# Optimization experiments

Measured on AMD Instinct MI355X. Metric: run time of the kernel, lower is better.

## Reference

```python
import jax, jax.numpy as jnp
import numpy as np

B = 524288
D_IN = 128
D_OUT = 128
MASK_DENSITY = 0.25  # fraction of DAG edges present


def setup_inputs() -> dict:
    key = jax.random.key(0)
    k = jax.random.split(key, 6)
    x0 = jax.random.normal(k[0], (B, D_IN), dtype=jnp.float32)
    x1 = jax.random.normal(k[1], (B, D_IN), dtype=jnp.float32)
    # weights ~ N(0, 0.1^2) as in torch.normal(mean=0, std=0.1)
    w0 = jax.random.normal(k[2], (D_OUT, D_IN), dtype=jnp.float32) * 0.1
    w1 = jax.random.normal(k[3], (D_OUT, D_IN), dtype=jnp.float32) * 0.1
    # binary DAG connectivity masks [out_dim, in_dims[i]]
    m0 = (jax.random.uniform(k[4], (D_OUT, D_IN)) < MASK_DENSITY).astype(jnp.float32)
    m1 = (jax.random.uniform(k[5], (D_OUT, D_IN)) < MASK_DENSITY).astype(jnp.float32)
    return {"x0": x0, "x1": x1, "w0": w0, "w1": w1, "m0": m0, "m1": m1}


def reference(x0, x1, w0, w1, m0, m1):
    # sum_i  x_i @ (W_i * M_i)^T   -> [B, out_dim]
    # (note: original module creates self.bias but never adds it in forward)
    out = jnp.einsum("bi,oi->bo", x0, w0 * m0)
    out = out + jnp.einsum("bi,oi->bo", x1, w1 * m1)
    return out
```

## Files before the change

kernel.cpp:

```cpp
#include <hip/hip_runtime.h>

typedef __attribute__((ext_vector_type(8))) short bf16x8;
typedef __attribute__((ext_vector_type(4))) float f32x4;

#define NBLK 512
#define NTHR 512
#define NT   32
#define DOUT 128

__device__ __forceinline__ unsigned short bf_rne(float x) {
  unsigned u = __builtin_bit_cast(unsigned, x);
  return (unsigned short)((u + 0x7FFFu + ((u >> 16) & 1u)) >> 16);
}
__device__ __forceinline__ void split2(float x, short& hi, short& lo) {
  unsigned u = __builtin_bit_cast(unsigned, x);
  float hf = __builtin_bit_cast(float, u & 0xFFFF0000u);
  hi = (short)(unsigned short)(u >> 16);
  lo = (short)bf_rne(x - hf);
}

__device__ __forceinline__ void gll16(const float* g, char* l) {
  __builtin_amdgcn_global_load_lds(
      (const __attribute__((address_space(1))) unsigned int*)g,
      (__attribute__((address_space(3))) unsigned int*)l, 16, 0, 0);
}

__global__ __launch_bounds__(NTHR, 2)
void dagmm(const float* __restrict__ x0, const float* __restrict__ x1,
           const float* __restrict__ w0, const float* __restrict__ w1,
           const float* __restrict__ m0, const float* __restrict__ m1,
           float* __restrict__ out)
{
  __shared__ __align__(16) char L[131072];

  const int t   = threadIdx.x;
  const int l   = t & 63;
  const int w   = t >> 6;
  const int l16 = l & 15;
  const int lq  = l >> 4;

  bf16x8 bhi[8], blo[8];
  {
    const int col = w * 16 + l16;
#pragma unroll
    for (int ks = 0; ks < 8; ++ks) {
      const int k0 = ks * 32 + lq * 8;
      const float* wp = (k0 < 128) ? (w0 + col * 128 + k0) : (w1 + col * 128 + (k0 - 128));
      const float* mp = (k0 < 128) ? (m0 + col * 128 + k0) : (m1 + col * 128 + (k0 - 128));
      float4 wa = *(const float4*)wp, wb = *(const float4*)(wp + 4);
      float4 ma = *(const float4*)mp, mb = *(const float4*)(mp + 4);
      float v[8] = {wa.x*ma.x, wa.y*ma.y, wa.z*ma.z, wa.w*ma.w,
                    wb.x*mb.x, wb.y*mb.y, wb.z*mb.z, wb.w*mb.w};
      bf16x8 hv, lv;
#pragma unroll
      for (int j = 0; j < 8; ++j) { short h, lo2; split2(v[j], h, lo2); hv[j] = h; lv[j] = lo2; }
      bhi[ks] = hv; blo[ks] = lv;
    }
  }

  const size_t Tbase = (size_t)blockIdx.x * (NT * 32);

  const float* xsrc = (l < 32) ? (x0 + l * 4) : (x1 + (l - 32) * 4);

#define ISSUE(ts, r)                                                        \
  {                                                                         \
    _Pragma("unroll")                                                       \
    for (int i = 0; i < 4; ++i) {                                           \
      const int row = w * 4 + i;                                            \
      const size_t grow = Tbase + (size_t)(ts) * 32 + row;                  \
      gll16(xsrc + grow * 128, L + (r) * 32768 + row * 1024);               \
    }                                                                       \
  }

  ISSUE(0, 0);
  ISSUE(1, 1);
  asm volatile("s_waitcnt vmcnt(4)" ::: "memory");

  const int rowS = w * 4 + (l >> 4);
  const int kf   = (l & 15) * 16;

  for (int tt = 0; tt < NT; ++tt) {
    const int r = tt & 1;

    {
      const char* Fb = L + r * 32768 + rowS * 1024 + kf * 4;
      float4 v0 = ((const float4*)Fb)[0], v1 = ((const float4*)Fb)[1];
      float4 v2 = ((const float4*)Fb)[2], v3 = ((const float4*)Fb)[3];
      const int rt = rowS >> 4;
#pragma unroll
      for (int q2 = 0; q2 < 2; ++q2) {
        float vv[8];
        if (q2 == 0) { vv[0]=v0.x; vv[1]=v0.y; vv[2]=v0.z; vv[3]=v0.w;
                       vv[4]=v1.x; vv[5]=v1.y; vv[6]=v1.z; vv[7]=v1.w; }
        else         { vv[0]=v2.x; vv[1]=v2.y; vv[2]=v2.z; vv[3]=v2.w;
                       vv[4]=v3.x; vv[5]=v3.y; vv[6]=v3.z; vv[7]=v3.w; }
        const int u  = (l & 15) * 2 + q2;
        const int ks = u >> 2, kq = u & 3;
        const int f  = rt * 8 + ks;
        const int slot = (kq * 16 + (rowS & 15)) ^ ks;
        bf16x8 hv, lv;
#pragma unroll
        for (int j = 0; j < 8; ++j) { short h, lo2; split2(vv[j], h, lo2); hv[j] = h; lv[j] = lo2; }
        char* bp = L + 65536 + r * 32768 + f * 1024 + slot * 16;
        *(bf16x8*)bp           = hv;
        *(bf16x8*)(bp + 16384) = lv;
      }
    }

    asm volatile("s_waitcnt lgkmcnt(0)" ::: "memory");
    __builtin_amdgcn_s_barrier();
    asm volatile("" ::: "memory");

    {
      const int ts = (tt + 2 < NT) ? (tt + 2) : (NT - 1);
      ISSUE(ts, r);
    }
    asm volatile("" ::: "memory");

    f32x4 acc[2];
    acc[0] = (f32x4){0.f, 0.f, 0.f, 0.f};
    acc[1] = (f32x4){0.f, 0.f, 0.f, 0.f};
#pragma unroll
    for (int ks = 0; ks < 8; ++ks) {
#pragma unroll
      for (int rt = 0; rt < 2; ++rt) {
        const char* bp = L + 65536 + r * 32768 + (rt * 8 + ks) * 1024 + ((l ^ ks) << 4);
        bf16x8 xh = *(const bf16x8*)bp;
        bf16x8 xl = *(const bf16x8*)(bp + 16384);
        acc[rt] = __builtin_amdgcn_mfma_f32_16x16x32_bf16(bhi[ks], xh, acc[rt], 0, 0, 0);
        acc[rt] = __builtin_amdgcn_mfma_f32_16x16x32_bf16(bhi[ks], xl, acc[rt], 0, 0, 0);
        acc[rt] = __builtin_amdgcn_mfma_f32_16x16x32_bf16(blo[ks], xh, acc[rt], 0, 0, 0);
      }
    }

#pragma unroll
    for (int rt = 0; rt < 2; ++rt) {
      const size_t row = Tbase + (size_t)tt * 32 + rt * 16 + l16;
      *(f32x4*)&out[row * DOUT + w * 16 + lq * 4] = acc[rt];
    }

    asm volatile("s_waitcnt vmcnt(6)" ::: "memory");
    __builtin_amdgcn_s_barrier();
    asm volatile("" ::: "memory");
  }
#undef ISSUE
}

extern "C" void kernel_launch(void* const* d_in, const int* in_sizes, int n_in,
                              void* d_out, int out_size, void* d_ws, size_t ws_size,
                              hipStream_t stream) {
  const float* x0 = (const float*)d_in[0];
  const float* x1 = (const float*)d_in[1];
  const float* w0 = (const float*)d_in[2];
  const float* w1 = (const float*)d_in[3];
  const float* m0 = (const float*)d_in[4];
  const float* m1 = (const float*)d_in[5];
  dagmm<<<NBLK, NTHR, 0, stream>>>(x0, x1, w0, w1, m0, m1, (float*)d_out);
}
```

Baseline: 175.5 us.

## Overlap next-tile bf16 split with current MFMA and drop a barrier

Result: slower. 188.6 us (+7.4%).

```diff
diff --git a/kernel.cpp b/kernel.cpp
--- a/kernel.cpp
+++ b/kernel.cpp
@@ -2,6 +2,7 @@
 
 typedef __attribute__((ext_vector_type(8))) short bf16x8;
 typedef __attribute__((ext_vector_type(4))) float f32x4;
+typedef __attribute__((ext_vector_type(2))) unsigned int u32x2;
 
 #define NBLK 512
 #define NTHR 512
@@ -72,64 +73,65 @@
     }                                                                       \
   }
 
+#define SPLIT(rr)                                                           \
+  {                                                                         \
+    const int rowS = w * 4 + (l >> 4);                                      \
+    const int v    = l & 15;                                                \
+    const char* Fb = L + (rr) * 32768 + rowS * 1024;                        \
+    char* Bh = L + 65536 + (rr) * 32768 + rowS * 512;                       \
+    _Pragma("unroll")                                                       \
+    for (int q = 0; q < 4; ++q) {                                           \
+      const int g = v + 16 * q;              \
+      float4 fv = *(const float4*)(Fb + g * 16);                            \
+      short h0,h1,h2,h3, e0,e1,e2,e3;                                       \
+      split2(fv.x, h0, e0); split2(fv.y, h1, e1);                           \
+      split2(fv.z, h2, e2); split2(fv.w, h3, e3);                           \
+      u32x2 hv, lv;                                                         \
+      hv[0] = (unsigned short)h0 | ((unsigned)(unsigned short)h1 << 16);    \
+      hv[1] = (unsigned short)h2 | ((unsigned)(unsigned short)h3 << 16);    \
+      lv[0] = (unsigned short)e0 | ((unsigned)(unsigned short)e1 << 16);    \
+      lv[1] = (unsigned short)e2 | ((unsigned)(unsigned short)e3 << 16);    \
+      const int ks = g >> 3, qq = (g & 7) >> 1, h = g & 1;                  \
+      const int off = ((ks * 64 + qq * 16) ^ ((rowS & 7) << 4)) + h * 8;    \
+      *(u32x2*)(Bh + off)         = hv;                                     \
+      *(u32x2*)(Bh + off + 16384) = lv;                                     \
+    }                                                                       \
+  }
+
   ISSUE(0, 0);
   ISSUE(1, 1);
   asm volatile("s_waitcnt vmcnt(4)" ::: "memory");
-
-  const int rowS = w * 4 + (l >> 4);
-  const int kf   = (l & 15) * 16;
+  SPLIT(0);
+  asm volatile("s_waitcnt lgkmcnt(0)" ::: "memory");
+  __builtin_amdgcn_s_barrier();
+  asm volatile("" ::: "memory");
 
   for (int tt = 0; tt < NT; ++tt) {
     const int r = tt & 1;
 
-    {
-      const char* Fb = L + r * 32768 + rowS * 1024 + kf * 4;
-      float4 v0 = ((const float4*)Fb)[0], v1 = ((const float4*)Fb)[1];
-      float4 v2 = ((const float4*)Fb)[2], v3 = ((const float4*)Fb)[3];
-      const int rt = rowS >> 4;
-#pragma unroll
-      for (int q2 = 0; q2 < 2; ++q2) {
-        float vv[8];
-        if (q2 == 0) { vv[0]=v0.x; vv[1]=v0.y; vv[2]=v0.z; vv[3]=v0.w;
-                       vv[4]=v1.x; vv[5]=v1.y; vv[6]=v1.z; vv[7]=v1.w; }
-        else         { vv[0]=v2.x; vv[1]=v2.y; vv[2]=v2.z; vv[3]=v2.w;
-                       vv[4]=v3.x; vv[5]=v3.y; vv[6]=v3.z; vv[7]=v3.w; }
-        const int u  = (l & 15) * 2 + q2;
-        const int ks = u >> 2, kq = u & 3;
-        const int f  = rt * 8 + ks;
-        const int slot = (kq * 16 + (rowS & 15)) ^ ks;
-        bf16x8 hv, lv;
-#pragma unroll
-        for (int j = 0; j < 8; ++j) { short h, lo2; split2(vv[j], h, lo2); hv[j] = h; lv[j] = lo2; }
-        char* bp = L + 65536 + r * 32768 + f * 1024 + slot * 16;
-        *(bf16x8*)bp           = hv;
-        *(bf16x8*)(bp + 16384) = lv;
-      }
-    }
+    { const int ts = (tt + 2 < NT) ? (tt + 2) : (NT - 1); ISSUE(ts, r); }
 
-    asm volatile("s_waitcnt lgkmcnt(0)" ::: "memory");
-    __builtin_amdgcn_s_barrier();
-    asm volatile("" ::: "memory");
+    asm volatile("s_waitcnt vmcnt(4)" ::: "memory");
 
-    {
-      const int ts = (tt + 2 < NT) ? (tt + 2) : (NT - 1);
-      ISSUE(ts, r);
-    }
-    asm volatile("" ::: "memory");
+    if (tt + 1 < NT) SPLIT(r ^ 1);
 
     f32x4 acc[2];
     acc[0] = (f32x4){0.f, 0.f, 0.f, 0.f};
     acc[1] = (f32x4){0.f, 0.f, 0.f, 0.f};
+    {
+      const char* Bb = L + 65536 + r * 32768;
 #pragma unroll
-    for (int ks = 0; ks < 8; ++ks) {
+      for (int ks = 0; ks < 8; ++ks) {
 #pragma unroll
-      for (int rt = 0; rt < 2; ++rt) {
-        const char* bp = L + 65536 + r * 32768 + (rt * 8 + ks) * 1024 + ((l ^ ks) << 4);
-        bf16x8 xh = *(const bf16x8*)bp;
-        bf16x8 xl = *(const bf16x8*)(bp + 16384);
-        acc[rt] = __builtin_amdgcn_mfma_f32_16x16x32_bf16(bhi[ks], xh, acc[rt], 0, 0, 0);
-        acc[rt] = __builtin_amdgcn_mfma_f32_16x16x32_bf16(bhi[ks], xl, acc[rt], 0, 0, 0);
-        acc[rt] = __builtin_amdgcn_mfma_f32_16x16x32_bf16(blo[ks], xh, acc[rt], 0, 0, 0);
+        for (int rt = 0; rt < 2; ++rt) {
+          const int rl  = rt * 16 + l16;
+          const int off = rl * 512 + ((ks * 64 + lq * 16) ^ ((rl & 7) << 4));
+          bf16x8 xh = *(const bf16x8*)(Bb + off);
+          bf16x8 xl = *(const bf16x8*)(Bb + off + 16384);
+          acc[rt] = __builtin_amdgcn_mfma_f32_16x16x32_bf16(bhi[ks], xh, acc[rt], 0, 0, 0);
+          acc[rt] = __builtin_amdgcn_mfma_f32_16x16x32_bf16(bhi[ks], xl, acc[rt], 0, 0, 0);
+          acc[rt] = __builtin_amdgcn_mfma_f32_16x16x32_bf16(blo[ks], xh, acc[rt], 0, 0, 0);
+        }
       }
     }
 
@@ -139,11 +141,12 @@
       *(f32x4*)&out[row * DOUT + w * 16 + lq * 4] = acc[rt];
     }
 
-    asm volatile("s_waitcnt vmcnt(6)" ::: "memory");
+    asm volatile("s_waitcnt lgkmcnt(0)" ::: "memory");
     __builtin_amdgcn_s_barrier();
     asm volatile("" ::: "memory");
   }
 #undef ISSUE
+#undef SPLIT
 }
 
 extern "C" void kernel_launch(void* const* d_in, const int* in_sizes, int n_in,
```

## Shrink row tile to 16, triple-buffer LDS, overlap bf16 split with MFMA

Applied to the files above, without the earlier changes.

Measured after the change: 219.7 us. 25.2% more time.

```diff
diff --git a/kernel.cpp b/kernel.cpp
--- a/kernel.cpp
+++ b/kernel.cpp
@@ -2,8 +2,9 @@
 
 typedef __attribute__((ext_vector_type(8))) short bf16x8;
 typedef __attribute__((ext_vector_type(4))) float f32x4;
+typedef __attribute__((ext_vector_type(2))) unsigned int u32x2;
 
-#define NBLK 512
+#define NBLK 1024
 #define NTHR 512
 #define NT   32
 #define DOUT 128
@@ -18,7 +19,9 @@
   hi = (short)(unsigned short)(u >> 16);
   lo = (short)bf_rne(x - hf);
 }
-
+__device__ __forceinline__ unsigned pk(short a, short b) {
+  return (unsigned)(unsigned short)a | ((unsigned)(unsigned short)b << 16);
+}
 __device__ __forceinline__ void gll16(const float* g, char* l) {
   __builtin_amdgcn_global_load_lds(
       (const __attribute__((address_space(1))) unsigned int*)g,
@@ -31,7 +34,7 @@
            const float* __restrict__ m0, const float* __restrict__ m1,
            float* __restrict__ out)
 {
-  __shared__ __align__(16) char L[131072];
+  __shared__ __align__(16) char L[49152];
 
   const int t   = threadIdx.x;
   const int l   = t & 63;
@@ -58,92 +61,100 @@
     }
   }
 
-  const size_t Tbase = (size_t)blockIdx.x * (NT * 32);
-
+  const size_t Tbase = (size_t)blockIdx.x * (NT * 16);
   const float* xsrc = (l < 32) ? (x0 + l * 4) : (x1 + (l - 32) * 4);
 
-#define ISSUE(ts, r)                                                        \
+#define ISSUE(ts, sl)                                                       \
   {                                                                         \
     _Pragma("unroll")                                                       \
-    for (int i = 0; i < 4; ++i) {                                           \
-      const int row = w * 4 + i;                                            \
-      const size_t grow = Tbase + (size_t)(ts) * 32 + row;                  \
-      gll16(xsrc + grow * 128, L + (r) * 32768 + row * 1024);               \
+    for (int i = 0; i < 2; ++i) {                                           \
+      const int row = w * 2 + i;                                            \
+      const size_t grow = Tbase + (size_t)(ts) * 16 + row;                  \
+      gll16(xsrc + grow * 128, L + (sl) * 16384 + row * 1024);              \
     }                                                                       \
   }
 
+  const int rrow = t >> 5;
+  const int k0   = (t & 31) * 4;
+  const int ksA  = k0 >> 5;
+  const int lamA = (rrow & 15) | (((k0 >> 3) & 3) << 4);
+  const int j2   = (k0 & 7) * 2;
+
+#define WRITEPH(sl)                                                         \
+  {                                                                         \
+    short h0,h1,h2,h3, e0,e1,e2,e3;                                         \
+    split2(ra.x, h0, e0); split2(ra.y, h1, e1);                             \
+    split2(ra.z, h2, e2); split2(ra.w, h3, e3);                             \
+    u32x2 hv, lv;                                                           \
+    hv[0] = pk(h0, h1); hv[1] = pk(h2, h3);                                 \
+    lv[0] = pk(e0, e1); lv[1] = pk(e2, e3);                                 \
+    char* p = L + (sl) * 16384 + ksA * 1024 + ((lamA ^ ksA) << 4) + j2;     \
+    *(u32x2*)p          = hv;                                               \
+    *(u32x2*)(p + 8192) = lv;                                               \
+    split2(rb.x, h0, e0); split2(rb.y, h1, e1);                             \
+    split2(rb.z, h2, e2); split2(rb.w, h3, e3);                             \
+    hv[0] = pk(h0, h1); hv[1] = pk(h2, h3);                                 \
+    lv[0] = pk(e0, e1); lv[1] = pk(e2, e3);                                 \
+    const int ksB = ksA + 4;                                                \
+    char* q = L + (sl) * 16384 + ksB * 1024 + ((lamA ^ ksB) << 4) + j2;     \
+    *(u32x2*)q          = hv;                                               \
+    *(u32x2*)(q + 8192) = lv;                                               \
+  }
+
+  float4 ra, rb;
+
   ISSUE(0, 0);
   ISSUE(1, 1);
-  asm volatile("s_waitcnt vmcnt(4)" ::: "memory");
-
-  const int rowS = w * 4 + (l >> 4);
-  const int kf   = (l & 15) * 16;
+  asm volatile("s_waitcnt vmcnt(2)" ::: "memory");
+  ra = *(const float4*)(L + rrow * 1024 + k0 * 4);
+  rb = *(const float4*)(L + rrow * 1024 + k0 * 4 + 512);
+  asm volatile("s_waitcnt lgkmcnt(0)" ::: "memory");
+  __builtin_amdgcn_s_barrier();
+  WRITEPH(0);
+  asm volatile("s_waitcnt lgkmcnt(0)" ::: "memory");
+  __builtin_amdgcn_s_barrier();
 
   for (int tt = 0; tt < NT; ++tt) {
-    const int r = tt & 1;
+    const int s0 = tt % 3, s1 = (tt + 1) % 3, s2 = (tt + 2) % 3;
+
+    if (tt + 2 < NT) {
+      ISSUE(tt + 2, s2);
+      asm volatile("s_waitcnt vmcnt(2)" ::: "memory");
+    } else {
+      asm volatile("s_waitcnt vmcnt(0)" ::: "memory");
+    }
+
+    if (tt + 1 < NT) {
+      ra = *(const float4*)(L + s1 * 16384 + rrow * 1024 + k0 * 4);
+      rb = *(const float4*)(L + s1 * 16384 + rrow * 1024 + k0 * 4 + 512);
+    }
+
+    f32x4 acc = (f32x4){0.f, 0.f, 0.f, 0.f};
+#pragma unroll
+    for (int ks = 0; ks < 8; ++ks) {
+      const char* bp = L + s0 * 16384 + ks * 1024 + ((l ^ ks) << 4);
+      bf16x8 xh = *(const bf16x8*)bp;
+      bf16x8 xl = *(const bf16x8*)(bp + 8192);
+      acc = __builtin_amdgcn_mfma_f32_16x16x32_bf16(bhi[ks], xh, acc, 0, 0, 0);
+      acc = __builtin_amdgcn_mfma_f32_16x16x32_bf16(bhi[ks], xl, acc, 0, 0, 0);
+      acc = __builtin_amdgcn_mfma_f32_16x16x32_bf16(blo[ks], xh, acc, 0, 0, 0);
+    }
 
     {
-      const char* Fb = L + r * 32768 + rowS * 1024 + kf * 4;
-      float4 v0 = ((const float4*)Fb)[0], v1 = ((const float4*)Fb)[1];
-      float4 v2 = ((const float4*)Fb)[2], v3 = ((const float4*)Fb)[3];
-      const int rt = rowS >> 4;
-#pragma unroll
-      for (int q2 = 0; q2 < 2; ++q2) {
-        float vv[8];
-        if (q2 == 0) { vv[0]=v0.x; vv[1]=v0.y; vv[2]=v0.z; vv[3]=v0.w;
-                       vv[4]=v1.x; vv[5]=v1.y; vv[6]=v1.z; vv[7]=v1.w; }
-        else         { vv[0]=v2.x; vv[1]=v2.y; vv[2]=v2.z; vv[3]=v2.w;
-                       vv[4]=v3.x; vv[5]=v3.y; vv[6]=v3.z; vv[7]=v3.w; }
-        const int u  = (l & 15) * 2 + q2;
-        const int ks = u >> 2, kq = u & 3;
-        const int f  = rt * 8 + ks;
-        const int slot = (kq * 16 + (rowS & 15)) ^ ks;
-        bf16x8 hv, lv;
-#pragma unroll
-        for (int j = 0; j < 8; ++j) { short h, lo2; split2(vv[j], h, lo2); hv[j] = h; lv[j] = lo2; }
-        char* bp = L + 65536 + r * 32768 + f * 1024 + slot * 16;
-        *(bf16x8*)bp           = hv;
-        *(bf16x8*)(bp + 16384) = lv;
-      }
+      const size_t row = Tbase + (size_t)tt * 16 + l16;
+      *(f32x4*)&out[row * DOUT + w * 16 + lq * 4] = acc;
     }
 
     asm volatile("s_waitcnt lgkmcnt(0)" ::: "memory");
     __builtin_amdgcn_s_barrier();
-    asm volatile("" ::: "memory");
 
-    {
-      const int ts = (tt + 2 < NT) ? (tt + 2) : (NT - 1);
-      ISSUE(ts, r);
-    }
-    asm volatile("" ::: "memory");
+    if (tt + 1 < NT) WRITEPH(s1);
 
-    f32x4 acc[2];
-    acc[0] = (f32x4){0.f, 0.f, 0.f, 0.f};
-    acc[1] = (f32x4){0.f, 0.f, 0.f, 0.f};
-#pragma unroll
-    for (int ks = 0; ks < 8; ++ks) {
-#pragma unroll
-      for (int rt = 0; rt < 2; ++rt) {
-        const char* bp = L + 65536 + r * 32768 + (rt * 8 + ks) * 1024 + ((l ^ ks) << 4);
-        bf16x8 xh = *(const bf16x8*)bp;
-        bf16x8 xl = *(const bf16x8*)(bp + 16384);
-        acc[rt] = __builtin_amdgcn_mfma_f32_16x16x32_bf16(bhi[ks], xh, acc[rt], 0, 0, 0);
-        acc[rt] = __builtin_amdgcn_mfma_f32_16x16x32_bf16(bhi[ks], xl, acc[rt], 0, 0, 0);
-        acc[rt] = __builtin_amdgcn_mfma_f32_16x16x32_bf16(blo[ks], xh, acc[rt], 0, 0, 0);
-      }
-    }
-
-#pragma unroll
-    for (int rt = 0; rt < 2; ++rt) {
-      const size_t row = Tbase + (size_t)tt * 32 + rt * 16 + l16;
-      *(f32x4*)&out[row * DOUT + w * 16 + lq * 4] = acc[rt];
-    }
-
-    asm volatile("s_waitcnt vmcnt(6)" ::: "memory");
+    asm volatile("s_waitcnt lgkmcnt(0)" ::: "memory");
     __builtin_amdgcn_s_barrier();
-    asm volatile("" ::: "memory");
   }
 #undef ISSUE
+#undef WRITEPH
 }
 
 extern "C" void kernel_launch(void* const* d_in, const int* in_sizes, int n_in,
```
